# Optimization experiments

Hardware: AMD Instinct MI355X
Metric: run time of the kernel (lower is better)

The kernel has to match this reference:

```python
import jax, jax.numpy as jnp
import numpy as np

NUM_HEADS = 16
N_WIRES = 8  # d_k == n_wires, hard-coded in QLayer


def quantum_heads(x, theta):
    """Exact closed form of the 8-wire circuit: RX-encode + trainable RX + CNOT ring + PauliZ.
    RX(x)RX(t)=RX(x+t); product state -> independent bits with E[(-1)^b_i]=cos(ang_i);
    CNOT ring permutes basis so final-bit XOR subsets give:
      <Z_0> = prod_{i=1..7} cos(ang_i);  <Z_w> = prod_{i=0..w} cos(ang_i) for w>=1.
    """
    B, S, E = x.shape
    ang = x.reshape(B, S, NUM_HEADS, N_WIRES) + theta          # composed RX angles
    c = jnp.cos(ang)                                            # [B,S,H,8]
    cp = jnp.cumprod(c, axis=-1)                                # prefix products
    z0 = jnp.prod(c[..., 1:], axis=-1, keepdims=True)           # wire 0
    z = jnp.concatenate([z0, cp[..., 1:]], axis=-1)             # [B,S,H,8]
    return z.reshape(B, S, E)


def reference(x, theta, W, b):
    B, S, E = x.shape
    d_k = N_WIRES
    proj = quantum_heads(x, theta)                              # q = k = v (same fn of x)
    h = proj.reshape(B, S, NUM_HEADS, d_k).transpose(0, 2, 1, 3)  # [B,H,S,d]
    scores = jnp.einsum('bhqd,bhkd->bhqk', h, h) / jnp.sqrt(jnp.float32(d_k))
    attn = jax.nn.softmax(scores, axis=-1)
    out = jnp.einsum('bhqk,bhkd->bhqd', attn, h)
    out = out.transpose(0, 2, 1, 3).reshape(B, S, E)
    return out @ W.T + b


def setup_inputs() -> dict:
    key = jax.random.key(0)
    k1, k2, k3 = jax.random.split(key, 3)
    B, S, E = 8, 1024, 128
    x = jax.random.normal(k1, (B, S, E), dtype=jnp.float32)
    theta = jax.random.normal(k2, (N_WIRES,), dtype=jnp.float32)
    W = jax.random.normal(k3, (E, E), dtype=jnp.float32) / np.float32(np.sqrt(E))
    b = jnp.zeros((E,), dtype=jnp.float32)
    return {"x": x, "theta": theta, "W": W, "b": b}
```

## Files before the change

kernel.cpp:

```cpp
#include <hip/hip_runtime.h>

#define NHEADS 16
#define NW 8
#define SEQ 1024
#define BATCH 8
#define EMB 128
#define PW 132

typedef _Float16 half2_t __attribute__((ext_vector_type(2)));
typedef _Float16 half4_t __attribute__((ext_vector_type(4)));
typedef _Float16 half8_t __attribute__((ext_vector_type(8)));
typedef float    f32x4   __attribute__((ext_vector_type(4)));

__device__ __forceinline__ half2_t pkrtz(float a, float b) {
    return __builtin_bit_cast(half2_t, __builtin_amdgcn_cvt_pkrtz(a, b));
}

#define KVT       8192
#define KVT_STR   1040
#define ONES_OFF  16512
#define ZERO_OFF  16520
#define SMEM_H    16544

__device__ __forceinline__ void qrow(const float* __restrict__ xp,
                                     const float* __restrict__ th, float* z) {
    float4 a = *reinterpret_cast<const float4*>(xp);
    float4 b = *reinterpret_cast<const float4*>(xp + 4);
    float c0 = __cosf(a.x + th[0]);
    float c1 = __cosf(a.y + th[1]);
    float c2 = __cosf(a.z + th[2]);
    float c3 = __cosf(a.w + th[3]);
    float c4 = __cosf(b.x + th[4]);
    float c5 = __cosf(b.y + th[5]);
    float c6 = __cosf(b.z + th[6]);
    float c7 = __cosf(b.w + th[7]);
    float u = c1 * c2;
    u *= c3; u *= c4; u *= c5; u *= c6; u *= c7;
    z[0] = u;
    z[1] = c0 * c1;
    z[2] = z[1] * c2;
    z[3] = z[2] * c3;
    z[4] = z[3] * c4;
    z[5] = z[4] * c5;
    z[6] = z[5] * c6;
    z[7] = z[6] * c7;
}

__global__ __launch_bounds__(256, 4) void qattn_mfma(
    const float* __restrict__ x,
    const float* __restrict__ theta,
    __fp16* __restrict__ P)
{
    __shared__ __align__(16) _Float16 smem[SMEM_H];
    const int t   = threadIdx.x;
    const int bid = blockIdx.x;
    const int qs  = bid & 7;
    const int bh  = bid >> 3;
    const int b   = bh >> 4, h = bh & 15;

    float th[8];
#pragma unroll
    for (int w = 0; w < 8; ++w) th[w] = theta[w];

#pragma unroll
    for (int i = 0; i < 4; ++i) {
        const int kl = t + 256 * i;
        float z[8];
        qrow(x + ((size_t)(b * SEQ + kl) * EMB + h * NW), th, z);
        half8_t hv;
#pragma unroll
        for (int d = 0; d < 8; ++d) hv[d] = (_Float16)z[d];
        *reinterpret_cast<half8_t*>(&smem[kl * 8]) = hv;
#pragma unroll
        for (int d = 0; d < 8; ++d) smem[KVT + d * KVT_STR + kl] = hv[d];
    }
    if (t < 8)              smem[ONES_OFF + t]     = (_Float16)1.0f;
    else if (t < 16)        smem[ZERO_OFF + t - 8] = (_Float16)0.0f;
    __syncthreads();

    const int lane = t & 63;
    const int wv   = t >> 6;
    const int q16  = lane & 15;
    const int qd   = lane >> 4;
    const int qbase = qs * 128 + wv * 32;

    const _Float16 QSh = (_Float16)0.51012924f;
    half8_t qfrag[2];
#pragma unroll
    for (int qi = 0; qi < 2; ++qi) {
        const _Float16* qp = (qd == 0)
            ? &smem[(qbase + qi * 16 + q16) * 8] : &smem[ZERO_OFF];
        half8_t qv = *reinterpret_cast<const half8_t*>(qp);
#pragma unroll
        for (int j = 0; j < 8; ++j) qv[j] = qv[j] * QSh;
        qfrag[qi] = qv;
    }

    const _Float16* ka = (qd == 0) ? &smem[q16 * 8]        : &smem[ZERO_OFF];
    const _Float16* kb = (qd == 0) ? &smem[(16 + q16) * 8] : &smem[ZERO_OFF];
    const int kstep = (qd == 0) ? 256 : 0;
    const _Float16* vp; int vstep;
    if (q16 < 8)       { vp = &smem[KVT + q16 * KVT_STR + qd * 8]; vstep = 32; }
    else if (q16 == 8) { vp = &smem[ONES_OFF]; vstep = 0; }
    else               { vp = &smem[ZERO_OFF]; vstep = 0; }

    const bool oddq = (qd & 1);
    const bool hiC  = (qd >= 2);
    const int  iA   = (q16 + (qd & 1) * 32 + (qd >> 1) * 16) * 4;
    const int  iB   = iA ^ 64;
    const int  lidx = (32 + q16) * 4;

    f32x4 oacc[2] = {{0.f, 0.f, 0.f, 0.f}, {0.f, 0.f, 0.f, 0.f}};
    const f32x4 zc = {0.f, 0.f, 0.f, 0.f};

    half8_t kA = *reinterpret_cast<const half8_t*>(ka);
    half8_t kB = *reinterpret_cast<const half8_t*>(kb);
    half8_t vA = *reinterpret_cast<const half8_t*>(vp);

    for (int kt = 0; kt < 32; ++kt) {
        ka += kstep; kb += kstep; vp += vstep;
        half8_t nkA = *reinterpret_cast<const half8_t*>(ka);
        half8_t nkB = *reinterpret_cast<const half8_t*>(kb);
        half8_t nvA = *reinterpret_cast<const half8_t*>(vp);

#pragma unroll
        for (int qi = 0; qi < 2; ++qi) {
            f32x4 c0 = __builtin_amdgcn_mfma_f32_16x16x32_f16(kA, qfrag[qi], zc, 0, 0, 0);
            f32x4 c1 = __builtin_amdgcn_mfma_f32_16x16x32_f16(kB, qfrag[qi], zc, 0, 0, 0);
            half2_t p0 = pkrtz(__builtin_amdgcn_exp2f(c0[0]), __builtin_amdgcn_exp2f(c0[1]));
            half2_t p1 = pkrtz(__builtin_amdgcn_exp2f(c0[2]), __builtin_amdgcn_exp2f(c0[3]));
            half2_t p2 = pkrtz(__builtin_amdgcn_exp2f(c1[0]), __builtin_amdgcn_exp2f(c1[1]));
            half2_t p3 = pkrtz(__builtin_amdgcn_exp2f(c1[2]), __builtin_amdgcn_exp2f(c1[3]));
            union { half2_t h; int i; } u0, u1, u2, u3;
            u0.h = p0; u1.h = p1; u2.h = p2; u3.h = p3;
            const int a0 = oddq ? u2.i : u0.i;
            const int a1 = oddq ? u3.i : u1.i;
            const int a2 = oddq ? u0.i : u2.i;
            const int a3 = oddq ? u1.i : u3.i;
            const int r0 = __builtin_amdgcn_ds_bpermute(iA, a0);
            const int r1 = __builtin_amdgcn_ds_bpermute(iA, a1);
            const int r2 = __builtin_amdgcn_ds_bpermute(iB, a2);
            const int r3 = __builtin_amdgcn_ds_bpermute(iB, a3);
            union { int i[4]; half8_t h; } bf;
            bf.i[0] = hiC ? r2 : r0;
            bf.i[1] = hiC ? r3 : r1;
            bf.i[2] = hiC ? r0 : r2;
            bf.i[3] = hiC ? r1 : r3;
            oacc[qi] = __builtin_amdgcn_mfma_f32_16x16x32_f16(vA, bf.h, oacc[qi], 0, 0, 0);
        }
        kA = nkA; kB = nkB; vA = nvA;
    }

#pragma unroll
    for (int qi = 0; qi < 2; ++qi) {
        f32x4 c = oacc[qi];
        const float lsum = __int_as_float(
            __builtin_amdgcn_ds_bpermute(lidx, __float_as_int(c[0])));
        const float inv = 1.0f / lsum;
        if (qd < 2) {
            half2_t u0 = pkrtz(c[0] * inv, c[1] * inv);
            half2_t u1 = pkrtz(c[2] * inv, c[3] * inv);
            half4_t o4; o4[0] = u0[0]; o4[1] = u0[1]; o4[2] = u1[0]; o4[3] = u1[1];
            const int row = b * SEQ + qbase + qi * 16 + q16;
            *reinterpret_cast<half4_t*>(
                reinterpret_cast<_Float16*>(P) + (size_t)row * EMB + h * NW + qd * 4) = o4;
        }
    }
}

__global__ __launch_bounds__(256, 4) void proj_out(
    const __fp16* __restrict__ P,
    const float* __restrict__ W,
    const float* __restrict__ bias,
    float* __restrict__ out)
{
    __shared__ float Pl[32 * PW];
    __shared__ float Wl[32 * PW];
    const int t     = threadIdx.x;
    const int row0  = blockIdx.x * 32;
    const int ecol0 = blockIdx.y * 32;

#pragma unroll
    for (int i = 0; i < 2; ++i) {
        const int g  = t + 256 * i;
        const int r  = g >> 4;
        const int c8 = (g & 15) * 8;
        half8_t hv = *reinterpret_cast<const half8_t*>(
            reinterpret_cast<const _Float16*>(P) + (size_t)(row0 + r) * EMB + c8);
        float4 v0 = make_float4((float)hv[0], (float)hv[1], (float)hv[2], (float)hv[3]);
        float4 v1 = make_float4((float)hv[4], (float)hv[5], (float)hv[6], (float)hv[7]);
        *reinterpret_cast<float4*>(&Pl[r * PW + c8])     = v0;
        *reinterpret_cast<float4*>(&Pl[r * PW + c8 + 4]) = v1;
    }
#pragma unroll
    for (int i = 0; i < 4; ++i) {
        const int g  = t + 256 * i;
        const int e  = g >> 5;
        const int k0 = (g & 31) * 4;
        *reinterpret_cast<float4*>(&Wl[e * PW + k0]) =
            *reinterpret_cast<const float4*>(W + (size_t)(ecol0 + e) * EMB + k0);
    }
    __syncthreads();

    const int rb = t >> 4;
    const int cb = t & 15;
    float acc00 = 0.f, acc01 = 0.f, acc10 = 0.f, acc11 = 0.f;
    for (int kk = 0; kk < EMB; kk += 4) {
        float4 a0 = *reinterpret_cast<const float4*>(&Pl[rb * PW + kk]);
        float4 a1 = *reinterpret_cast<const float4*>(&Pl[(rb + 16) * PW + kk]);
        float4 w0 = *reinterpret_cast<const float4*>(&Wl[cb * PW + kk]);
        float4 w1 = *reinterpret_cast<const float4*>(&Wl[(cb + 16) * PW + kk]);
        acc00 = fmaf(a0.x, w0.x, acc00); acc00 = fmaf(a0.y, w0.y, acc00);
        acc00 = fmaf(a0.z, w0.z, acc00); acc00 = fmaf(a0.w, w0.w, acc00);
        acc01 = fmaf(a0.x, w1.x, acc01); acc01 = fmaf(a0.y, w1.y, acc01);
        acc01 = fmaf(a0.z, w1.z, acc01); acc01 = fmaf(a0.w, w1.w, acc01);
        acc10 = fmaf(a1.x, w0.x, acc10); acc10 = fmaf(a1.y, w0.y, acc10);
        acc10 = fmaf(a1.z, w0.z, acc10); acc10 = fmaf(a1.w, w0.w, acc10);
        acc11 = fmaf(a1.x, w1.x, acc11); acc11 = fmaf(a1.y, w1.y, acc11);
        acc11 = fmaf(a1.z, w1.z, acc11); acc11 = fmaf(a1.w, w1.w, acc11);
    }

    const float b0 = bias[ecol0 + cb], b1 = bias[ecol0 + cb + 16];
    out[(size_t)(row0 + rb) * EMB + ecol0 + cb]           = acc00 + b0;
    out[(size_t)(row0 + rb) * EMB + ecol0 + cb + 16]      = acc01 + b1;
    out[(size_t)(row0 + rb + 16) * EMB + ecol0 + cb]      = acc10 + b0;
    out[(size_t)(row0 + rb + 16) * EMB + ecol0 + cb + 16] = acc11 + b1;
}

extern "C" void kernel_launch(void* const* d_in, const int* in_sizes, int n_in,
                              void* d_out, int out_size, void* d_ws, size_t ws_size,
                              hipStream_t stream)
{
    const float* x     = (const float*)d_in[0];
    const float* theta = (const float*)d_in[1];
    const float* W     = (const float*)d_in[2];
    const float* bias  = (const float*)d_in[3];
    float* out = (float*)d_out;

    __fp16* P = (__fp16*)d_ws;

    qattn_mfma<<<128 * 8, 256, 0, stream>>>(x, theta, P);
    proj_out<<<dim3(BATCH * SEQ / 32, EMB / 32), 256, 0, stream>>>(P, W, bias, out);
}
```

Baseline: 92.78 us.

## Replace FP32 output projection with FP16 MFMA projection and W pre-cast kernel

The scalar-FMA LDS-tiled output projection is replaced by a kernel that loads fp16 attention output and an fp16 copy of W directly into registers and uses 16x16x32 f16 MFMA instructions. A small extra kernel converts W to fp16 into workspace each call. This removes the LDS staging and FP32 FMA work in the projection, but adds a launch and lowers W precision to fp16.

```diff
diff --git a/kernel.cpp b/kernel.cpp
--- a/kernel.cpp
+++ b/kernel.cpp
@@ -5,7 +5,6 @@
 #define SEQ 1024
 #define BATCH 8
 #define EMB 128
-#define PW 132
 
 typedef _Float16 half2_t __attribute__((ext_vector_type(2)));
 typedef _Float16 half4_t __attribute__((ext_vector_type(4)));
@@ -168,63 +167,54 @@
     }
 }
 
-__global__ __launch_bounds__(256, 4) void proj_out(
-    const __fp16* __restrict__ P,
-    const float* __restrict__ W,
+__global__ __launch_bounds__(256) void wcast(
+    const float* __restrict__ W, _Float16* __restrict__ Wh)
+{
+    const int g = (blockIdx.x * 256 + threadIdx.x) * 4;
+    float4 v = *reinterpret_cast<const float4*>(W + g);
+    half4_t h;
+    h[0] = (_Float16)v.x; h[1] = (_Float16)v.y;
+    h[2] = (_Float16)v.z; h[3] = (_Float16)v.w;
+    *reinterpret_cast<half4_t*>(Wh + g) = h;
+}
+
+__global__ __launch_bounds__(256) void proj_mfma(
+    const __fp16* __restrict__ Pv,
+    const _Float16* __restrict__ Wh,
     const float* __restrict__ bias,
     float* __restrict__ out)
 {
-    __shared__ float Pl[32 * PW];
-    __shared__ float Wl[32 * PW];
-    const int t     = threadIdx.x;
-    const int row0  = blockIdx.x * 32;
-    const int ecol0 = blockIdx.y * 32;
-
-#pragma unroll
-    for (int i = 0; i < 2; ++i) {
-        const int g  = t + 256 * i;
-        const int r  = g >> 4;
-        const int c8 = (g & 15) * 8;
-        half8_t hv = *reinterpret_cast<const half8_t*>(
-            reinterpret_cast<const _Float16*>(P) + (size_t)(row0 + r) * EMB + c8);
-        float4 v0 = make_float4((float)hv[0], (float)hv[1], (float)hv[2], (float)hv[3]);
-        float4 v1 = make_float4((float)hv[4], (float)hv[5], (float)hv[6], (float)hv[7]);
-        *reinterpret_cast<float4*>(&Pl[r * PW + c8])     = v0;
-        *reinterpret_cast<float4*>(&Pl[r * PW + c8 + 4]) = v1;
-    }
-#pragma unroll
-    for (int i = 0; i < 4; ++i) {
-        const int g  = t + 256 * i;
-        const int e  = g >> 5;
-        const int k0 = (g & 31) * 4;
-        *reinterpret_cast<float4*>(&Wl[e * PW + k0]) =
-            *reinterpret_cast<const float4*>(W + (size_t)(ecol0 + e) * EMB + k0);
-    }
-    __syncthreads();
-
-    const int rb = t >> 4;
-    const int cb = t & 15;
-    float acc00 = 0.f, acc01 = 0.f, acc10 = 0.f, acc11 = 0.f;
-    for (int kk = 0; kk < EMB; kk += 4) {
-        float4 a0 = *reinterpret_cast<const float4*>(&Pl[rb * PW + kk]);
-        float4 a1 = *reinterpret_cast<const float4*>(&Pl[(rb + 16) * PW + kk]);
-        float4 w0 = *reinterpret_cast<const float4*>(&Wl[cb * PW + kk]);
-        float4 w1 = *reinterpret_cast<const float4*>(&Wl[(cb + 16) * PW + kk]);
-        acc00 = fmaf(a0.x, w0.x, acc00); acc00 = fmaf(a0.y, w0.y, acc00);
-        acc00 = fmaf(a0.z, w0.z, acc00); acc00 = fmaf(a0.w, w0.w, acc00);
-        acc01 = fmaf(a0.x, w1.x, acc01); acc01 = fmaf(a0.y, w1.y, acc01);
-        acc01 = fmaf(a0.z, w1.z, acc01); acc01 = fmaf(a0.w, w1.w, acc01);
-        acc10 = fmaf(a1.x, w0.x, acc10); acc10 = fmaf(a1.y, w0.y, acc10);
-        acc10 = fmaf(a1.z, w0.z, acc10); acc10 = fmaf(a1.w, w0.w, acc10);
-        acc11 = fmaf(a1.x, w1.x, acc11); acc11 = fmaf(a1.y, w1.y, acc11);
-        acc11 = fmaf(a1.z, w1.z, acc11); acc11 = fmaf(a1.w, w1.w, acc11);
-    }
-
-    const float b0 = bias[ecol0 + cb], b1 = bias[ecol0 + cb + 16];
-    out[(size_t)(row0 + rb) * EMB + ecol0 + cb]           = acc00 + b0;
-    out[(size_t)(row0 + rb) * EMB + ecol0 + cb + 16]      = acc01 + b1;
-    out[(size_t)(row0 + rb + 16) * EMB + ecol0 + cb]      = acc10 + b0;
-    out[(size_t)(row0 + rb + 16) * EMB + ecol0 + cb + 16] = acc11 + b1;
+    const _Float16* P = reinterpret_cast<const _Float16*>(Pv);
+    const int t    = threadIdx.x;
+    const int lane = t & 63;
+    const int wv   = t >> 6;
+    const int n16  = lane & 15;
+    const int qd   = lane >> 4;
+    const int row0 = blockIdx.x * 16;
+    const int col0 = wv * 32;
+
+    half8_t a[4];
+#pragma unroll
+    for (int kb = 0; kb < 4; ++kb)
+        a[kb] = *reinterpret_cast<const half8_t*>(
+            P + (size_t)(row0 + n16) * EMB + kb * 32 + qd * 8);
+
+    const f32x4 zc = {0.f, 0.f, 0.f, 0.f};
+#pragma unroll
+    for (int et = 0; et < 2; ++et) {
+        const int e = col0 + et * 16 + n16;
+        f32x4 acc = zc;
+#pragma unroll
+        for (int kb = 0; kb < 4; ++kb) {
+            half8_t bfr = *reinterpret_cast<const half8_t*>(
+                Wh + (size_t)e * EMB + kb * 32 + qd * 8);
+            acc = __builtin_amdgcn_mfma_f32_16x16x32_f16(a[kb], bfr, acc, 0, 0, 0);
+        }
+        const float bv = bias[e];
+#pragma unroll
+        for (int r = 0; r < 4; ++r)
+            out[(size_t)(row0 + qd * 4 + r) * EMB + e] = acc[r] + bv;
+    }
 }
 
 extern "C" void kernel_launch(void* const* d_in, const int* in_sizes, int n_in,
@@ -237,8 +227,10 @@
     const float* bias  = (const float*)d_in[3];
     float* out = (float*)d_out;
 
-    __fp16* P = (__fp16*)d_ws;
-
-    qattn_mfma<<<128 * 8, 256, 0, stream>>>(x, theta, P);
-    proj_out<<<dim3(BATCH * SEQ / 32, EMB / 32), 256, 0, stream>>>(P, W, bias, out);
-}
+    __fp16*   Pw = (__fp16*)d_ws;
+    _Float16* Wh = (_Float16*)((char*)d_ws + (size_t)BATCH * SEQ * EMB * 2);
+
+    wcast<<<16, 256, 0, stream>>>(W, Wh);
+    qattn_mfma<<<128 * 8, 256, 0, stream>>>(x, theta, Pw);
+    proj_mfma<<<BATCH * SEQ / 16, 256, 0, stream>>>(Pw, Wh, bias, out);
+}
```

Result: no change. 92.84 us (+0.1%).
